# Kernel optimization log

Hardware: AMD Instinct MI355X
Metric: run time of the kernel (lower is better)

The kernel has to match this reference:

```python
import jax, jax.numpy as jnp
import numpy as np
from jax import lax

EPS = 1e-5
N_CROPS = 501
CROP_W = 500
RF = 65          # temporal receptive field
KS = 15          # conv1 kernel size
POOL = 3


def _bn(x, g, b, m, v, axis=1):
    shp = [1] * x.ndim
    shp[axis] = -1
    inv = g.reshape(shp) / jnp.sqrt(v.reshape(shp) + EPS)
    return (x - m.reshape(shp)) * inv + b.reshape(shp)


def setup_inputs() -> dict:
    key = jax.random.key(0)
    ks = jax.random.split(key, 16)
    B, C_IN, CH, T = 16, 1, 22, 1001
    F = 36
    OUT = 4
    FLAT = F * 43  # 1548 (corrected fc in_features; repo constant 504 is inconsistent)
    d = {
        "x": jax.random.normal(ks[0], (B, C_IN, CH, T), jnp.float32),
        # temporal conv [1,65]
        "w_t": jax.random.normal(ks[1], (F, 1, 1, RF), jnp.float32) * 0.1,
        "b_t": jax.random.normal(ks[2], (F,), jnp.float32) * 0.1,
        "bn_t_g": jax.random.uniform(ks[3], (F,), jnp.float32, 0.5, 1.5),
        "bn_t_b": jax.random.normal(ks[4], (F,), jnp.float32) * 0.1,
        "bn_t_m": jax.random.normal(ks[5], (F,), jnp.float32) * 0.1,
        "bn_t_v": jax.random.uniform(ks[6], (F,), jnp.float32, 0.5, 1.5),
        # spatial conv [22,1]
        "w_s": jax.random.normal(ks[7], (F, F, CH, 1), jnp.float32) * 0.05,
        "b_s": jax.random.normal(ks[8], (F,), jnp.float32) * 0.1,
        "bn_s_g": jax.random.uniform(ks[9], (F,), jnp.float32, 0.5, 1.5),
        "bn_s_b": jax.random.normal(ks[10], (F,), jnp.float32) * 0.1,
        "bn_s_m": jax.random.normal(ks[11], (F,), jnp.float32) * 0.1,
        "bn_s_v": jax.random.uniform(ks[12], (F,), jnp.float32, 0.5, 1.5),
        # conv1 [1,15] (as 1-D conv over time)
        "w_c": jax.random.normal(ks[13], (F, F, KS), jnp.float32) * 0.05,
        "b_c": jax.random.normal(ks[14], (F,), jnp.float32) * 0.1,
        "bn_c_g": jnp.ones((F,), jnp.float32),
        "bn_c_b": jnp.zeros((F,), jnp.float32),
        "bn_c_m": jnp.zeros((F,), jnp.float32),
        "bn_c_v": jnp.ones((F,), jnp.float32),
        # fc
        "w_fc": jax.random.normal(ks[15], (OUT, FLAT), jnp.float32) * 0.02,
        "b_fc": jnp.zeros((OUT,), jnp.float32),
    }
    return d


def reference(x, w_t, b_t, bn_t_g, bn_t_b, bn_t_m, bn_t_v,
              w_s, b_s, bn_s_g, bn_s_b, bn_s_m, bn_s_v,
              w_c, b_c, bn_c_g, bn_c_b, bn_c_m, bn_c_v,
              w_fc, b_fc):
    B = x.shape[0]
    F = w_t.shape[0]
    OUT = b_fc.shape[0]

    # temporal + spatial conv/BN/ELU are shift-invariant -> compute once over full T
    h = lax.conv_general_dilated(x, w_t, (1, 1), 'VALID',
                                 dimension_numbers=('NCHW', 'OIHW', 'NCHW'))
    h = h + b_t[None, :, None, None]                       # [B,36,22,937]
    h = jax.nn.elu(_bn(h, bn_t_g, bn_t_b, bn_t_m, bn_t_v))
    h = lax.conv_general_dilated(h, w_s, (1, 1), 'VALID',
                                 dimension_numbers=('NCHW', 'OIHW', 'NCHW'))
    h = h + b_s[None, :, None, None]                       # [B,36,1,937]
    h = jax.nn.elu(_bn(h, bn_s_g, bn_s_b, bn_s_m, bn_s_v))
    h = h[:, :, 0, :]                                      # [B,36,937]

    TW = CROP_W - RF + 1  # 436: temporal width of each crop after temporal conv

    def crop_logits(i):
        sl = lax.dynamic_slice_in_dim(h, i, TW, axis=2)    # [B,36,436]
        p1 = sl[:, :, :435].reshape(B, F, 145, POOL).mean(-1)  # avgpool1 -> [B,36,145]
        c = lax.conv_general_dilated(p1, w_c, (1,), 'VALID',
                                     dimension_numbers=('NCH', 'OIH', 'NCH'))
        c = c + b_c[None, :, None]                          # [B,36,131]
        c = jax.nn.elu(_bn(c, bn_c_g, bn_c_b, bn_c_m, bn_c_v))
        p2 = c[:, :, :129].reshape(B, F, 43, POOL).mean(-1)  # avgpool2 -> [B,36,43]
        flat = p2.reshape(B, -1)                            # [B,1548]
        return flat @ w_fc.T + b_fc                         # [B,OUT]

    def step(acc, i):
        return acc + crop_logits(i), None

    init = jnp.zeros((B, OUT), x.dtype)
    total, _ = lax.scan(step, init, jnp.arange(N_CROPS))
    return total / N_CROPS
```

## Files before the change

kernel.cpp:

```cpp
#include <hip/hip_runtime.h>

#define EPS 1e-5f
#define B 16
#define CH 22
#define T_IN 1001
#define F 36
#define RF 65
#define T1 937
#define FC 792
#define TW 64
#define NTW 15
#define UN 885
#define PSPAN 304
#define KS 15
#define GN 295
#define WN 129
#define M43 43
#define BF 576
#define FLAT 1548

#define H2_OFF  0
#define EP_OFF  539712
#define WTT_OFF 4617792
#define WST_OFF 4620132
#define WCT_OFF 4648644
#define BN_OFF  4668084

__device__ __forceinline__ float elu_f(float v) {
    return v > 0.f ? v : (__expf(v) - 1.f);
}

__global__ __launch_bounds__(256) void k_prep(
    const float* __restrict__ w_t, const float* __restrict__ w_s,
    const float* __restrict__ w_c,
    const float* __restrict__ b_t, const float* __restrict__ g_t,
    const float* __restrict__ be_t,const float* __restrict__ m_t,
    const float* __restrict__ v_t,
    const float* __restrict__ b_s, const float* __restrict__ g_s,
    const float* __restrict__ be_s,const float* __restrict__ m_s,
    const float* __restrict__ v_s,
    const float* __restrict__ b_c, const float* __restrict__ g_c,
    const float* __restrict__ be_c,const float* __restrict__ m_c,
    const float* __restrict__ v_c, const float* __restrict__ b_fc,
    float* __restrict__ wtT, float* __restrict__ wsT,
    float* __restrict__ wcT, float* __restrict__ bnz,
    float* __restrict__ out)
{
    int i = blockIdx.x * 256 + threadIdx.x;
    if (i < F * RF)     { int k = i / F,  fi = i % F; wtT[i] = w_t[fi * RF + k]; }
    if (i < FC * F)     { int fc = i / F, fo = i % F; wsT[i] = w_s[fo * FC + fc]; }
    if (i < F * KS * F) { int fk = i / F, fo = i % F; int f = fk / KS, k = fk % KS;
                          wcT[i] = w_c[(fo * F + f) * KS + k]; }
    if (i < F) {
        float s1 = g_t[i] * rsqrtf(v_t[i] + EPS);
        bnz[i]          = s1;
        bnz[F + i]      = (b_t[i] - m_t[i]) * s1 + be_t[i];
        float s2 = g_s[i] * rsqrtf(v_s[i] + EPS);
        bnz[2 * F + i]  = s2;
        bnz[3 * F + i]  = (b_s[i] - m_s[i]) * s2 + be_s[i];
        float s3 = g_c[i] * rsqrtf(v_c[i] + EPS);
        bnz[4 * F + i]  = s3;
        bnz[5 * F + i]  = (b_c[i] - m_c[i]) * s3 + be_c[i];
    }
    if (i < B * 4) out[i] = b_fc[i & 3];
}

__global__ __launch_bounds__(768) void k_front(
    const float* __restrict__ x, const float* __restrict__ wtT,
    const float* __restrict__ wsT, const float* __restrict__ bnz,
    float* __restrict__ h2)
{
    __shared__ float Ls[4 * F * TW];
    const int tid = threadIdx.x;
    const int lane = tid & 63;
    const int w = __builtin_amdgcn_readfirstlane(tid >> 6);
    const int fi0 = 3 * w;
    const int b = blockIdx.y;
    const int t0 = blockIdx.x * TW;
    int t = t0 + lane;
    int tc = t < T1 ? t : (T1 - 1);

    float acc[F];
    #pragma unroll
    for (int j = 0; j < F; ++j) acc[j] = 0.f;

    const float s10 = bnz[fi0],     o10 = bnz[F + fi0];
    const float s11 = bnz[fi0 + 1], o11 = bnz[F + fi0 + 1];
    const float s12 = bnz[fi0 + 2], o12 = bnz[F + fi0 + 2];

    for (int ch = 0; ch < CH; ++ch) {
        const float* xp = x + (b * CH + ch) * T_IN + tc;
        float ha = 0.f, hb = 0.f, hc = 0.f;
        #pragma unroll 13
        for (int k = 0; k < RF; ++k) {
            float xv = xp[k];
            const float* wr = wtT + k * F + fi0;
            ha += xv * wr[0];
            hb += xv * wr[1];
            hc += xv * wr[2];
        }
        float e0 = elu_f(ha * s10 + o10);
        float e1 = elu_f(hb * s11 + o11);
        float e2 = elu_f(hc * s12 + o12);
        const float* w0 = wsT + ((fi0 + 0) * CH + ch) * F;
        const float* w1 = wsT + ((fi0 + 1) * CH + ch) * F;
        const float* w2 = wsT + ((fi0 + 2) * CH + ch) * F;
        #pragma unroll
        for (int fo = 0; fo < F; ++fo)
            acc[fo] += e0 * w0[fo] + e1 * w1[fo] + e2 * w2[fo];
    }

    const int r = w & 3;
    float* row = &Ls[(size_t)r * (F * TW)];
    if (w < 4) {
        #pragma unroll
        for (int fo = 0; fo < F; ++fo) row[fo * TW + lane] = acc[fo];
    }
    __syncthreads();
    if (w >= 4 && w < 8) {
        #pragma unroll
        for (int fo = 0; fo < F; ++fo) row[fo * TW + lane] += acc[fo];
    }
    __syncthreads();
    if (w >= 8) {
        #pragma unroll
        for (int fo = 0; fo < F; ++fo) row[fo * TW + lane] += acc[fo];
    }
    __syncthreads();

    for (int i = tid; i < F * TW; i += 768) {
        float s = Ls[i] + Ls[F * TW + i] + Ls[2 * F * TW + i] + Ls[3 * F * TW + i];
        int fo = i / TW, tl = i % TW;
        int tg = t0 + tl;
        if (tg < T1) {
            float s2 = bnz[2 * F + fo], o2 = bnz[3 * F + fo];
            h2[(b * F + fo) * T1 + tg] = elu_f(s * s2 + o2);
        }
    }
}

__global__ __launch_bounds__(256) void k_qconv(
    const float* __restrict__ h2, const float* __restrict__ wcT,
    float* __restrict__ Ep)
{
    __shared__ float Ps[5 * PSPAN];
    const int tid = threadIdx.x;
    const int slice = blockIdx.y, b = blockIdx.z;
    const int u0 = blockIdx.x * 256;
    const int f_base = slice < 4 ? slice * 5 : 20 + (slice - 4) * 4;
    const int nf     = slice < 4 ? 5 : 4;

    for (int i = tid; i < nf * PSPAN; i += 256) {
        int fl = i / PSPAN, j = i % PSPAN;
        const float* hr = h2 + (size_t)(b * F + f_base + fl) * T1;
        int s = u0 + j;
        int s0 = s     < T1 - 1 ? s     : T1 - 1;
        int s1 = s + 1 < T1 - 1 ? s + 1 : T1 - 1;
        int s2 = s + 2 < T1 - 1 ? s + 2 : T1 - 1;
        Ps[i] = (hr[s0] + hr[s1] + hr[s2]) * (1.f / 3.f);
    }
    __syncthreads();

    const int lu = tid;

    float acc[F];
    #pragma unroll
    for (int j = 0; j < F; ++j) acc[j] = 0.f;

    for (int fl = 0; fl < nf; ++fl) {
        const int pb = fl * PSPAN + lu;
        #pragma unroll 5
        for (int k = 0; k < KS; ++k) {
            float pv = Ps[pb + 3 * k];
            const float* wr = wcT + ((f_base + fl) * KS + k) * F;
            #pragma unroll
            for (int j = 0; j < F; ++j) acc[j] += pv * wr[j];
        }
    }

    int u_g = u0 + lu;
    if (u_g < UN) {
        #pragma unroll
        for (int j = 0; j < F; ++j)
            Ep[(((size_t)slice * B + b) * F + j) * UN + u_g] = acc[j];
    }
}

__global__ __launch_bounds__(256) void k_wins(
    const float* __restrict__ Ep, const float* __restrict__ bnz,
    const float* __restrict__ w_fc, float* __restrict__ out)
{
    __shared__ float Es[UN];
    __shared__ float G[GN];
    __shared__ float Ws[WN];
    __shared__ float Sm[M43];
    const int tid = threadIdx.x;
    const int bf = blockIdx.x;
    const int b = bf / F, f = bf % F;
    const float sc = bnz[4 * F + f];
    const float oc = bnz[5 * F + f];
    for (int i = tid; i < UN; i += 256) {
        float s = 0.f;
        #pragma unroll
        for (int sl = 0; sl < 8; ++sl)
            s += Ep[((size_t)sl * BF + bf) * UN + i];
        Es[i] = elu_f(s * sc + oc);
    }
    __syncthreads();
    for (int q = tid; q < GN; q += 256)
        G[q] = Es[3 * q] + Es[3 * q + 1] + Es[3 * q + 2];
    __syncthreads();
    if (tid < WN) {
        float a = 0.f;
        for (int q = tid; q < tid + 167; ++q) a += G[q];
        Ws[tid] = a;
    }
    __syncthreads();
    if (tid < M43)
        Sm[tid] = (Ws[3 * tid] + Ws[3 * tid + 1] + Ws[3 * tid + 2]) * (1.f / 3.f);
    __syncthreads();
    if (tid < 4) {
        const float* wr = w_fc + tid * FLAT + f * M43;
        float a = 0.f;
        #pragma unroll 43
        for (int m = 0; m < M43; ++m) a += Sm[m] * wr[m];
        atomicAdd(&out[b * 4 + tid], a * (1.f / 501.f));
    }
}

extern "C" void kernel_launch(void* const* d_in, const int* in_sizes, int n_in,
                              void* d_out, int out_size, void* d_ws, size_t ws_size,
                              hipStream_t stream) {
    const float* x    = (const float*)d_in[0];
    const float* w_t  = (const float*)d_in[1];
    const float* b_t  = (const float*)d_in[2];
    const float* g_t  = (const float*)d_in[3];
    const float* be_t = (const float*)d_in[4];
    const float* m_t  = (const float*)d_in[5];
    const float* v_t  = (const float*)d_in[6];
    const float* w_s  = (const float*)d_in[7];
    const float* b_s  = (const float*)d_in[8];
    const float* g_s  = (const float*)d_in[9];
    const float* be_s = (const float*)d_in[10];
    const float* m_s  = (const float*)d_in[11];
    const float* v_s  = (const float*)d_in[12];
    const float* w_c  = (const float*)d_in[13];
    const float* b_c  = (const float*)d_in[14];
    const float* g_c  = (const float*)d_in[15];
    const float* be_c = (const float*)d_in[16];
    const float* m_c  = (const float*)d_in[17];
    const float* v_c  = (const float*)d_in[18];
    const float* w_fc = (const float*)d_in[19];
    const float* b_fc = (const float*)d_in[20];

    float* ws  = (float*)d_ws;
    float* h2  = ws + H2_OFF;
    float* Ep  = ws + EP_OFF;
    float* wtT = ws + WTT_OFF;
    float* wsT = ws + WST_OFF;
    float* wcT = ws + WCT_OFF;
    float* bnz = ws + BN_OFF;
    float* out = (float*)d_out;

    k_prep<<<dim3(112), 256, 0, stream>>>(
        w_t, w_s, w_c, b_t, g_t, be_t, m_t, v_t,
        b_s, g_s, be_s, m_s, v_s, b_c, g_c, be_c, m_c, v_c, b_fc,
        wtT, wsT, wcT, bnz, out);

    k_front<<<dim3(NTW, B), 768, 0, stream>>>(x, wtT, wsT, bnz, h2);
    k_qconv<<<dim3(4, 8, B), 256, 0, stream>>>(h2, wcT, Ep);
    k_wins<<<dim3(BF), 256, 0, stream>>>(Ep, bnz, w_fc, out);
}
```

Before: 188.0 us.

## Split front kernel over channel groups and defer spatial BN/ELU into qconv

The front kernel now splits the 22 EEG channels into 3 groups across a new grid dimension, with 4 waves each handling 9 temporal filters, and writes partial spatial-conv sums. The BN+ELU of the spatial stage moves into k_qconv, which sums the three partials while loading. k_qconv is also split into 12 filter slices of 3 instead of 8. This raises block count and parallelism for the front stage, at the cost of extra partial-sum traffic and workspace, and of recomputing ELU per pooled tap.

```diff
diff --git a/kernel.cpp b/kernel.cpp
--- a/kernel.cpp
+++ b/kernel.cpp
@@ -10,6 +10,8 @@
 #define FC 792
 #define TW 64
 #define NTW 15
+#define CSPL 3
+#define QSPL 12
 #define UN 885
 #define PSPAN 304
 #define KS 15
@@ -19,12 +21,12 @@
 #define BF 576
 #define FLAT 1548
 
-#define H2_OFF  0
-#define EP_OFF  539712
-#define WTT_OFF 4617792
-#define WST_OFF 4620132
-#define WCT_OFF 4648644
-#define BN_OFF  4668084
+#define H2P_OFF 0
+#define EP_OFF  1619136
+#define WTP_OFF 7736256
+#define WSP_OFF 7738596
+#define WCT_OFF 7767108
+#define BN_OFF  7786548
 
 __device__ __forceinline__ float elu_f(float v) {
     return v > 0.f ? v : (__expf(v) - 1.f);
@@ -42,15 +44,23 @@
     const float* __restrict__ b_c, const float* __restrict__ g_c,
     const float* __restrict__ be_c,const float* __restrict__ m_c,
     const float* __restrict__ v_c, const float* __restrict__ b_fc,
-    float* __restrict__ wtT, float* __restrict__ wsT,
+    float* __restrict__ wtP, float* __restrict__ wsP,
     float* __restrict__ wcT, float* __restrict__ bnz,
     float* __restrict__ out)
 {
     int i = blockIdx.x * 256 + threadIdx.x;
-    if (i < F * RF)     { int k = i / F,  fi = i % F; wtT[i] = w_t[fi * RF + k]; }
-    if (i < FC * F)     { int fc = i / F, fo = i % F; wsT[i] = w_s[fo * FC + fc]; }
-    if (i < F * KS * F) { int fk = i / F, fo = i % F; int f = fk / KS, k = fk % KS;
-                          wcT[i] = w_c[(fo * F + f) * KS + k]; }
+    if (i < 4 * RF * 9) {
+        int jj = i % 9, k = (i / 9) % RF, g = i / (9 * RF);
+        wtP[i] = w_t[(9 * g + jj) * RF + k];
+    }
+    if (i < 4 * CH * F * 9) {
+        int jj = i % 9, fo = (i / 9) % F, ch = (i / (9 * F)) % CH, g = i / (9 * F * CH);
+        wsP[i] = w_s[(fo * F + 9 * g + jj) * CH + ch];
+    }
+    if (i < F * KS * F) {
+        int fk = i / F, fo = i % F; int f = fk / KS, k = fk % KS;
+        wcT[i] = w_c[(fo * F + f) * KS + k];
+    }
     if (i < F) {
         float s1 = g_t[i] * rsqrtf(v_t[i] + EPS);
         bnz[i]          = s1;
@@ -65,99 +75,110 @@
     if (i < B * 4) out[i] = b_fc[i & 3];
 }
 
-__global__ __launch_bounds__(768) void k_front(
-    const float* __restrict__ x, const float* __restrict__ wtT,
-    const float* __restrict__ wsT, const float* __restrict__ bnz,
-    float* __restrict__ h2)
-{
-    __shared__ float Ls[4 * F * TW];
+__global__ __launch_bounds__(256) void k_front(
+    const float* __restrict__ x, const float* __restrict__ wtP,
+    const float* __restrict__ wsP, const float* __restrict__ bnz,
+    float* __restrict__ h2p)
+{
+    __shared__ float Ls[2 * F * TW];
     const int tid = threadIdx.x;
     const int lane = tid & 63;
-    const int w = __builtin_amdgcn_readfirstlane(tid >> 6);
-    const int fi0 = 3 * w;
-    const int b = blockIdx.y;
+    const int g = __builtin_amdgcn_readfirstlane(tid >> 6);
+    const int chg = blockIdx.y, b = blockIdx.z;
+    const int ch0 = (chg == 0) ? 0 : (8 + (chg - 1) * 7);
+    const int nch = (chg == 0) ? 8 : 7;
     const int t0 = blockIdx.x * TW;
     int t = t0 + lane;
     int tc = t < T1 ? t : (T1 - 1);
 
+    float s1v[9], o1v[9];
+    #pragma unroll
+    for (int jj = 0; jj < 9; ++jj) {
+        s1v[jj] = bnz[9 * g + jj];
+        o1v[jj] = bnz[F + 9 * g + jj];
+    }
+
     float acc[F];
     #pragma unroll
     for (int j = 0; j < F; ++j) acc[j] = 0.f;
 
-    const float s10 = bnz[fi0],     o10 = bnz[F + fi0];
-    const float s11 = bnz[fi0 + 1], o11 = bnz[F + fi0 + 1];
-    const float s12 = bnz[fi0 + 2], o12 = bnz[F + fi0 + 2];
-
-    for (int ch = 0; ch < CH; ++ch) {
+    for (int c = 0; c < nch; ++c) {
+        const int ch = ch0 + c;
         const float* xp = x + (b * CH + ch) * T_IN + tc;
-        float ha = 0.f, hb = 0.f, hc = 0.f;
-        #pragma unroll 13
+        float h[9];
+        #pragma unroll
+        for (int jj = 0; jj < 9; ++jj) h[jj] = 0.f;
+
+        #pragma unroll 5
         for (int k = 0; k < RF; ++k) {
             float xv = xp[k];
-            const float* wr = wtT + k * F + fi0;
-            ha += xv * wr[0];
-            hb += xv * wr[1];
-            hc += xv * wr[2];
-        }
-        float e0 = elu_f(ha * s10 + o10);
-        float e1 = elu_f(hb * s11 + o11);
-        float e2 = elu_f(hc * s12 + o12);
-        const float* w0 = wsT + ((fi0 + 0) * CH + ch) * F;
-        const float* w1 = wsT + ((fi0 + 1) * CH + ch) * F;
-        const float* w2 = wsT + ((fi0 + 2) * CH + ch) * F;
-        #pragma unroll
-        for (int fo = 0; fo < F; ++fo)
-            acc[fo] += e0 * w0[fo] + e1 * w1[fo] + e2 * w2[fo];
-    }
-
-    const int r = w & 3;
-    float* row = &Ls[(size_t)r * (F * TW)];
-    if (w < 4) {
+            const float* wr = wtP + (g * RF + k) * 9;
+            #pragma unroll
+            for (int jj = 0; jj < 9; ++jj) h[jj] += xv * wr[jj];
+        }
+
+        float e[9];
+        #pragma unroll
+        for (int jj = 0; jj < 9; ++jj)
+            e[jj] = elu_f(h[jj] * s1v[jj] + o1v[jj]);
+
+        const float* wq = wsP + ((size_t)(g * CH + ch) * F) * 9;
+        #pragma unroll
+        for (int fo = 0; fo < F; ++fo) {
+            const float* wrr = wq + fo * 9;
+            float a = acc[fo];
+            #pragma unroll
+            for (int jj = 0; jj < 9; ++jj) a += e[jj] * wrr[jj];
+            acc[fo] = a;
+        }
+    }
+
+    float* row = &Ls[(size_t)(g & 1) * (F * TW)];
+    if (g < 2) {
         #pragma unroll
         for (int fo = 0; fo < F; ++fo) row[fo * TW + lane] = acc[fo];
     }
     __syncthreads();
-    if (w >= 4 && w < 8) {
+    if (g >= 2) {
         #pragma unroll
         for (int fo = 0; fo < F; ++fo) row[fo * TW + lane] += acc[fo];
     }
     __syncthreads();
-    if (w >= 8) {
-        #pragma unroll
-        for (int fo = 0; fo < F; ++fo) row[fo * TW + lane] += acc[fo];
-    }
-    __syncthreads();
-
-    for (int i = tid; i < F * TW; i += 768) {
-        float s = Ls[i] + Ls[F * TW + i] + Ls[2 * F * TW + i] + Ls[3 * F * TW + i];
+
+    for (int i = tid; i < F * TW; i += 256) {
+        float s = Ls[i] + Ls[F * TW + i];
         int fo = i / TW, tl = i % TW;
         int tg = t0 + tl;
-        if (tg < T1) {
-            float s2 = bnz[2 * F + fo], o2 = bnz[3 * F + fo];
-            h2[(b * F + fo) * T1 + tg] = elu_f(s * s2 + o2);
-        }
+        if (tg < T1)
+            h2p[(((size_t)chg * B + b) * F + fo) * T1 + tg] = s;
     }
 }
 
 __global__ __launch_bounds__(256) void k_qconv(
-    const float* __restrict__ h2, const float* __restrict__ wcT,
-    float* __restrict__ Ep)
-{
-    __shared__ float Ps[5 * PSPAN];
+    const float* __restrict__ h2p, const float* __restrict__ wcT,
+    const float* __restrict__ bnz, float* __restrict__ Ep)
+{
+    __shared__ float Ps[3 * PSPAN];
     const int tid = threadIdx.x;
     const int slice = blockIdx.y, b = blockIdx.z;
     const int u0 = blockIdx.x * 256;
-    const int f_base = slice < 4 ? slice * 5 : 20 + (slice - 4) * 4;
-    const int nf     = slice < 4 ? 5 : 4;
-
-    for (int i = tid; i < nf * PSPAN; i += 256) {
+    const int f_base = slice * 3;
+
+    for (int i = tid; i < 3 * PSPAN; i += 256) {
         int fl = i / PSPAN, j = i % PSPAN;
-        const float* hr = h2 + (size_t)(b * F + f_base + fl) * T1;
-        int s = u0 + j;
-        int s0 = s     < T1 - 1 ? s     : T1 - 1;
-        int s1 = s + 1 < T1 - 1 ? s + 1 : T1 - 1;
-        int s2 = s + 2 < T1 - 1 ? s + 2 : T1 - 1;
-        Ps[i] = (hr[s0] + hr[s1] + hr[s2]) * (1.f / 3.f);
+        int f = f_base + fl;
+        float s2 = bnz[2 * F + f], o2 = bnz[3 * F + f];
+        const float* p0 = h2p + ((size_t)(0 * B + b) * F + f) * T1;
+        const float* p1 = h2p + ((size_t)(1 * B + b) * F + f) * T1;
+        const float* p2 = h2p + ((size_t)(2 * B + b) * F + f) * T1;
+        float a = 0.f;
+        #pragma unroll
+        for (int d = 0; d < 3; ++d) {
+            int s = u0 + j + d; if (s > T1 - 1) s = T1 - 1;
+            float q = p0[s] + p1[s] + p2[s];
+            a += elu_f(q * s2 + o2);
+        }
+        Ps[i] = a * (1.f / 3.f);
     }
     __syncthreads();
 
@@ -167,7 +188,8 @@
     #pragma unroll
     for (int j = 0; j < F; ++j) acc[j] = 0.f;
 
-    for (int fl = 0; fl < nf; ++fl) {
+    #pragma unroll
+    for (int fl = 0; fl < 3; ++fl) {
         const int pb = fl * PSPAN + lu;
         #pragma unroll 5
         for (int k = 0; k < KS; ++k) {
@@ -202,7 +224,7 @@
     for (int i = tid; i < UN; i += 256) {
         float s = 0.f;
         #pragma unroll
-        for (int sl = 0; sl < 8; ++sl)
+        for (int sl = 0; sl < QSPL; ++sl)
             s += Ep[((size_t)sl * BF + bf) * UN + i];
         Es[i] = elu_f(s * sc + oc);
     }
@@ -254,10 +276,10 @@
     const float* b_fc = (const float*)d_in[20];
 
     float* ws  = (float*)d_ws;
-    float* h2  = ws + H2_OFF;
+    float* h2p = ws + H2P_OFF;
     float* Ep  = ws + EP_OFF;
-    float* wtT = ws + WTT_OFF;
-    float* wsT = ws + WST_OFF;
+    float* wtP = ws + WTP_OFF;
+    float* wsP = ws + WSP_OFF;
     float* wcT = ws + WCT_OFF;
     float* bnz = ws + BN_OFF;
     float* out = (float*)d_out;
@@ -265,9 +287,9 @@
     k_prep<<<dim3(112), 256, 0, stream>>>(
         w_t, w_s, w_c, b_t, g_t, be_t, m_t, v_t,
         b_s, g_s, be_s, m_s, v_s, b_c, g_c, be_c, m_c, v_c, b_fc,
-        wtT, wsT, wcT, bnz, out);
-
-    k_front<<<dim3(NTW, B), 768, 0, stream>>>(x, wtT, wsT, bnz, h2);
-    k_qconv<<<dim3(4, 8, B), 256, 0, stream>>>(h2, wcT, Ep);
+        wtP, wsP, wcT, bnz, out);
+
+    k_front<<<dim3(NTW, CSPL, B), 256, 0, stream>>>(x, wtP, wsP, bnz, h2p);
+    k_qconv<<<dim3(4, QSPL, B), 256, 0, stream>>>(h2p, wcT, bnz, Ep);
     k_wins<<<dim3(BF), 256, 0, stream>>>(Ep, bnz, w_fc, out);
 }
```

Result: slower. 207.3 us (+10.3%).
